# Optimization experiments

Hardware: AMD Instinct MI355X
Metric: run time of the kernel (lower is better)

## Reference

```python
import jax, jax.numpy as jnp
import numpy as np
from jax import lax

EMBED = 64


def setup_inputs() -> dict:
    key = jax.random.key(0)
    ks = jax.random.split(key, 5)
    b, l, v, e, h = 256, 1024, 96, 64, 256
    x = jax.random.randint(ks[0], (b, l), 0, v, dtype=jnp.int64)
    hidden = jnp.zeros((b, h), dtype=jnp.float32)
    # xavier-uniform-like init (scale by fan sums)
    emb = jax.random.normal(ks[1], (v, e), dtype=jnp.float32) * 0.1
    W_ih = jax.random.normal(ks[2], (e + h, h), dtype=jnp.float32) * (1.0 / np.sqrt(e + h))
    b_ih = jnp.zeros((h,), dtype=jnp.float32)
    W_ho = jax.random.normal(ks[3], (h, v), dtype=jnp.float32) * (1.0 / np.sqrt(h))
    b_ho = jnp.zeros((v,), dtype=jnp.float32)
    return {"x": x, "hidden": hidden, "emb": emb, "W_ih": W_ih, "b_ih": b_ih,
            "W_ho": W_ho, "b_ho": b_ho}


def reference(x, hidden, emb, W_ih, b_ih, W_ho, b_ho):
    # x: [b, l] int indices; hidden: [b, h]
    x_embed = emb[x]                      # [b, l, e]
    Wx, Wh = W_ih[:EMBED], W_ih[EMBED:]   # split cat([x, h]) @ W_ih
    # precompute input projections for all timesteps (batched GEMM)
    xproj = jnp.einsum('ble,eh->blh', x_embed, Wx) + b_ih  # [b, l, h]

    def step(h_prev, xp_t):
        h_t = jnp.tanh(xp_t + h_prev @ Wh)  # [b, h]
        return h_t, h_t

    final_hidden, hs = lax.scan(step, hidden, xproj.transpose(1, 0, 2))  # hs: [l, b, h]
    hs = hs.transpose(1, 0, 2)                     # [b, l, h]
    logits = jnp.einsum('blh,hv->blv', hs, W_ho) + b_ho  # [b, l, v]
    return logits, final_hidden
```

## Files before the change

kernel.cpp:

```cpp
#include <hip/hip_runtime.h>
#include <hip/hip_bf16.h>

#define Lv 1024
#define Vv 96
#define Ev 64
#define Hv 256
#define ROWS 16
#define HOFF (256 * 1024 * 96)
#define EPAD 72
#define HB 4096

typedef __attribute__((ext_vector_type(8))) short bf16x8;
typedef __attribute__((ext_vector_type(4))) float f32x4;
typedef __attribute__((ext_vector_type(2))) unsigned int u32x2;

__device__ __forceinline__ unsigned short f2b(float f) {
  unsigned u = __builtin_bit_cast(unsigned, f);
  return (unsigned short)((u + 0x7fffu + ((u >> 16) & 1u)) >> 16);
}
__device__ __forceinline__ unsigned cvtpk_bf16(float lo, float hi) {
  unsigned r;
  asm("v_cvt_pk_bf16_f32 %0, %1, %2" : "=v"(r) : "v"(lo), "v"(hi));
  return r;
}
__device__ __forceinline__ float fast_tanh(float x) {
  float e = __builtin_amdgcn_exp2f(x * 2.885390081777927f);
  return 1.0f - 2.0f * __builtin_amdgcn_rcpf(e + 1.0f);
}
__device__ __forceinline__ void step_barrier() {
  asm volatile("s_waitcnt lgkmcnt(0)\n\ts_barrier" ::: "memory");
  __builtin_amdgcn_sched_barrier(0);
}

__global__ void detect_i64(const int* __restrict__ x, int* __restrict__ flag) {
  if (threadIdx.x == 0 && blockIdx.x == 0) {
    int ok = 1;
    for (int i = 0; i < 64; ++i) ok &= (x[2 * i + 1] == 0);
    *flag = ok;
  }
}

__global__ __launch_bounds__(512, 2) void rnn8t(
    const int* __restrict__ x, const float* __restrict__ h0,
    const float* __restrict__ emb, const float* __restrict__ W_ih,
    const float* __restrict__ b_ih, float* __restrict__ out,
    unsigned short* __restrict__ hs, const int* __restrict__ flagp) {
  const int tid = threadIdx.x;
  const int w = tid >> 6, ln = tid & 63, lm = ln & 15, g = ln >> 4;
  const int r0 = blockIdx.x * ROWS;

  __shared__ __attribute__((aligned(16))) unsigned short s_h[2 * HB];
  __shared__ __attribute__((aligned(16))) unsigned short s_emb[Vv * EPAD];
  __shared__ unsigned char s_x[Lv * ROWS];

  const int flag = *flagp;

  for (int idx = tid; idx < Vv * Ev; idx += 512)
    s_emb[(idx >> 6) * EPAD + (idx & 63)] = f2b(emb[idx]);
  for (int idx = tid; idx < ROWS * Hv; idx += 512) {
    int b_ = idx >> 8, hd = idx & 255;
    s_h[HB + b_ * 256 + ((((hd >> 3) ^ (b_ & 7)) << 3) | (hd & 7))] =
        f2b(h0[(r0 + b_) * Hv + hd]);
  }
  for (int idx = tid; idx < ROWS * Lv; idx += 512) {
    int t = idx >> 4, row = idx & 15;
    long long src = (long long)(r0 + row) * Lv + t;
    int v = flag ? x[2 * src] : x[src];
    s_x[t * ROWS + row] = (unsigned char)v;
  }

  bf16x8 wh[2][8], wx[2][2];
  f32x4 bihv[2];
#pragma unroll
  for (int nt = 0; nt < 2; ++nt) {
    const int n = 32 * w + 16 * nt + lm;
#pragma unroll
    for (int kf = 0; kf < 8; ++kf)
#pragma unroll
      for (int i = 0; i < 8; ++i)
        wh[nt][kf][i] = (short)f2b(W_ih[(Ev + 32 * kf + 8 * g + i) * Hv + n]);
#pragma unroll
    for (int kf = 0; kf < 2; ++kf)
#pragma unroll
      for (int i = 0; i < 8; ++i)
        wx[nt][kf][i] = (short)f2b(W_ih[(32 * kf + 8 * g + i) * Hv + n]);
    bihv[nt] = *(const f32x4*)&b_ih[32 * w + 16 * nt + 4 * g];
  }

  const unsigned short* ra[8];
#pragma unroll
  for (int kf = 0; kf < 8; ++kf)
    ra[kf] = &s_h[lm * 256 + (((4 * kf + g) ^ (lm & 7)) << 3)];
  unsigned short* wa[2];
#pragma unroll
  for (int nt = 0; nt < 2; ++nt)
    wa[nt] = &s_h[lm * 256 + (((4 * w + 2 * nt + (g >> 1)) ^ (lm & 7)) << 3) +
                  ((g & 1) << 2)];
  unsigned short* hp = hs + (size_t)(r0 + lm) * 0 ;
  hp = hs + (size_t)(r0 + lm) * 256 + 32 * w + 4 * g;

  __syncthreads();

  bf16x8 ef0, ef1;
  int xi_n;
  {
    int xi0 = s_x[lm];
    const unsigned short* ep = &s_emb[xi0 * EPAD + 8 * g];
    ef0 = *(const bf16x8*)ep;
    ef1 = *(const bf16x8*)(ep + 32);
    xi_n = s_x[ROWS + lm];
  }

#define STEP(TT, RB, WB, LAST)                                                    \
  do {                                                                            \
    bf16x8 af[8];                                                                 \
    _Pragma("unroll") for (int kf = 0; kf < 8; ++kf)                              \
        af[kf] = *(const bf16x8*)(ra[kf] + (RB));                                 \
    f32x4 aA0 = bihv[0], aA1 = bihv[1];                                           \
    f32x4 aB0 = {0.f, 0.f, 0.f, 0.f}, aB1 = {0.f, 0.f, 0.f, 0.f};                 \
    aA0 = __builtin_amdgcn_mfma_f32_16x16x32_bf16(wx[0][0], ef0, aA0, 0, 0, 0);   \
    aA1 = __builtin_amdgcn_mfma_f32_16x16x32_bf16(wx[1][0], ef0, aA1, 0, 0, 0);   \
    aB0 = __builtin_amdgcn_mfma_f32_16x16x32_bf16(wx[0][1], ef1, aB0, 0, 0, 0);   \
    aB1 = __builtin_amdgcn_mfma_f32_16x16x32_bf16(wx[1][1], ef1, aB1, 0, 0, 0);   \
    _Pragma("unroll") for (int kf = 0; kf < 4; ++kf) {                            \
      aA0 = __builtin_amdgcn_mfma_f32_16x16x32_bf16(wh[0][kf], af[kf], aA0, 0, 0, 0); \
      aA1 = __builtin_amdgcn_mfma_f32_16x16x32_bf16(wh[1][kf], af[kf], aA1, 0, 0, 0); \
    }                                                                             \
    _Pragma("unroll") for (int kf = 4; kf < 8; ++kf) {                            \
      aB0 = __builtin_amdgcn_mfma_f32_16x16x32_bf16(wh[0][kf], af[kf], aB0, 0, 0, 0); \
      aB1 = __builtin_amdgcn_mfma_f32_16x16x32_bf16(wh[1][kf], af[kf], aB1, 0, 0, 0); \
    }                                                                             \
    {                                      \
      const unsigned short* ep = &s_emb[xi_n * EPAD + 8 * g];                     \
      ef0 = *(const bf16x8*)ep;                                                   \
      ef1 = *(const bf16x8*)(ep + 32);                                            \
      int tn = ((TT) + 2 < Lv) ? (TT) + 2 : (Lv - 1);                             \
      xi_n = s_x[tn * ROWS + lm];                                                 \
    }                                                                             \
    float h0v = fast_tanh(aA0[0] + aB0[0]), h1v = fast_tanh(aA0[1] + aB0[1]);     \
    float h2v = fast_tanh(aA0[2] + aB0[2]), h3v = fast_tanh(aA0[3] + aB0[3]);     \
    float h4v = fast_tanh(aA1[0] + aB1[0]), h5v = fast_tanh(aA1[1] + aB1[1]);     \
    float h6v = fast_tanh(aA1[2] + aB1[2]), h7v = fast_tanh(aA1[3] + aB1[3]);     \
    u32x2 p0, p1;                                                                 \
    p0[0] = cvtpk_bf16(h0v, h1v);                                                 \
    p0[1] = cvtpk_bf16(h2v, h3v);                                                 \
    p1[0] = cvtpk_bf16(h4v, h5v);                                                 \
    p1[1] = cvtpk_bf16(h6v, h7v);                                                 \
    *(u32x2*)(wa[0] + (WB)) = p0;                                                 \
    *(u32x2*)(wa[1] + (WB)) = p1;                                                 \
    *(u32x2*)hp = p0;                                           \
    *(u32x2*)(hp + 16) = p1;                                    \
    hp += 256 * 256;                                                              \
    if (LAST) {                                                                   \
      float* fo = out + HOFF + (size_t)(r0 + lm) * Hv + 32 * w + 4 * g;           \
      *(f32x4*)fo = (f32x4){h0v, h1v, h2v, h3v};                                  \
      *(f32x4*)(fo + 16) = (f32x4){h4v, h5v, h6v, h7v};                           \
    }                                                                             \
    step_barrier();                                                               \
  } while (0)

  STEP(0, HB, 0, 0);
  for (int t = 1; t < Lv - 1; t += 2) {
    STEP(t, 0, HB, 0);
    STEP(t + 1, HB, 0, 0);
  }
  STEP(Lv - 1, 0, HB, 1);
#undef STEP
}

__global__ __launch_bounds__(512, 2) void logits_gemm(
    const unsigned short* __restrict__ hs, const float* __restrict__ W_ho,
    const float* __restrict__ b_ho, float* __restrict__ out) {
  const int tid = threadIdx.x;
  const int w = tid >> 6, ln = tid & 63, lm = ln & 15, g = ln >> 4;
  const int tg = blockIdx.x >> 2, bg = blockIdx.x & 3;

  __shared__ __attribute__((aligned(16))) unsigned short s_who[3072 * 8];
  for (int f = tid; f < 3072; f += 512) {
    int vt = f >> 9, kf = (f >> 6) & 7, lane = f & 63;
    int k0 = 32 * kf + 8 * (lane >> 4), v = 16 * vt + (lane & 15);
    bf16x8 fr;
#pragma unroll
    for (int i = 0; i < 8; ++i) fr[i] = (short)f2b(W_ho[(k0 + i) * Vv + v]);
    *(bf16x8*)&s_who[f * 8] = fr;
  }
  __syncthreads();

  const int bt = w & 3, vg = w >> 2;
  const int b0 = bg * 64 + bt * 16;
  const int j0 = vg * 3;
  float bb[3];
#pragma unroll
  for (int jj = 0; jj < 3; ++jj) bb[jj] = b_ho[16 * (j0 + jj) + lm];

#pragma unroll
  for (int tt = 0; tt < 4; ++tt) {
    const int t = tg * 4 + tt;
    const unsigned short* hpb =
        hs + (size_t)t * (256 * 256) + (b0 + lm) * 256 + 8 * g;
    f32x4 acc[3];
#pragma unroll
    for (int jj = 0; jj < 3; ++jj)
      acc[jj] = (f32x4){bb[jj], bb[jj], bb[jj], bb[jj]};
#pragma unroll
    for (int kf = 0; kf < 8; ++kf) {
      bf16x8 af = *(const bf16x8*)(hpb + 32 * kf);
#pragma unroll
      for (int jj = 0; jj < 3; ++jj) {
        bf16x8 bw = *(const bf16x8*)&s_who[(((j0 + jj) * 8 + kf) * 64 + ln) * 8];
        acc[jj] =
            __builtin_amdgcn_mfma_f32_16x16x32_bf16(af, bw, acc[jj], 0, 0, 0);
      }
    }
#pragma unroll
    for (int jj = 0; jj < 3; ++jj)
#pragma unroll
      for (int rr = 0; rr < 4; ++rr)
        out[(size_t)(b0 + 4 * g + rr) * (Lv * Vv) + (size_t)t * Vv +
            16 * (j0 + jj) + lm] = acc[jj][rr];
  }
}

__global__ __launch_bounds__(512, 2) void rnn8(
    const int* __restrict__ x, const float* __restrict__ h0,
    const float* __restrict__ emb, const float* __restrict__ W_ih,
    const float* __restrict__ b_ih, const float* __restrict__ W_ho,
    const float* __restrict__ b_ho, float* __restrict__ out,
    const int* __restrict__ flagp) {
  const int tid = threadIdx.x;
  const int w = tid >> 6, ln = tid & 63, lm = ln & 15, g = ln >> 4;
  const int r0 = blockIdx.x * ROWS;

  __shared__ __attribute__((aligned(16))) unsigned short s_emb[Vv * EPAD];
  __shared__ __attribute__((aligned(16))) unsigned short s_h[2 * HB];
  __shared__ unsigned char s_x[Lv * ROWS];

  const int flag = *flagp;

  for (int idx = tid; idx < Vv * Ev; idx += 512)
    s_emb[(idx >> 6) * EPAD + (idx & 63)] = f2b(emb[idx]);
  for (int idx = tid; idx < ROWS * Hv; idx += 512) {
    int m = idx >> 8, nn = idx & 255;
    s_h[HB + (m << 8) + ((((nn >> 3) ^ (m & 7)) << 3) | (nn & 7))] =
        f2b(h0[(r0 + m) * Hv + nn]);
  }
  for (int idx = tid; idx < ROWS * Lv; idx += 512) {
    int row = idx >> 10, t = idx & 1023;
    long long src = (long long)(r0 + row) * Lv + t;
    int v = flag ? x[2 * src] : x[src];
    s_x[t * ROWS + row] = (unsigned char)v;
  }

  bf16x8 wh[2][8], wx[2][2], who[8];
  float bih[2], bhov = 0.0f;
#pragma unroll
  for (int nt = 0; nt < 2; ++nt) {
    const int n = 32 * w + 16 * nt + lm;
    bih[nt] = b_ih[n];
#pragma unroll
    for (int kf = 0; kf < 8; ++kf)
#pragma unroll
      for (int i = 0; i < 8; ++i)
        wh[nt][kf][i] = (short)f2b(W_ih[(Ev + 32 * kf + 8 * g + i) * Hv + n]);
#pragma unroll
    for (int kf = 0; kf < 2; ++kf)
#pragma unroll
      for (int i = 0; i < 8; ++i)
        wx[nt][kf][i] = (short)f2b(W_ih[(32 * kf + 8 * g + i) * Hv + n]);
  }
  if (w < 6) {
    const int n = 16 * w + lm;
    bhov = b_ho[n];
#pragma unroll
    for (int kf = 0; kf < 8; ++kf)
#pragma unroll
      for (int i = 0; i < 8; ++i)
        who[kf][i] = (short)f2b(W_ho[(32 * kf + 8 * g + i) * Vv + n]);
  }

  const unsigned short* ra[8];
#pragma unroll
  for (int kf = 0; kf < 8; ++kf)
    ra[kf] = &s_h[(lm << 8) + (((4 * kf + g) ^ (lm & 7)) << 3)];
  unsigned short* wa[8];
#pragma unroll
  for (int nt = 0; nt < 2; ++nt)
#pragma unroll
    for (int rr = 0; rr < 4; ++rr) {
      int m = 4 * g + rr, n = 32 * w + 16 * nt + lm;
      wa[nt * 4 + rr] = &s_h[(m << 8) + ((((n >> 3) ^ (m & 7)) << 3) | (n & 7))];
    }
  float* ob[4] = {out, out, out, out};
  if (w < 6) {
#pragma unroll
    for (int rr = 0; rr < 4; ++rr)
      ob[rr] = out + (size_t)(r0 + 4 * g + rr) * (Lv * Vv) + 16 * w + lm;
  }

  __syncthreads();

  bf16x8 ef0, ef1;
  {
    int xi = s_x[lm];
    const unsigned short* ep = &s_emb[xi * EPAD + 8 * g];
    ef0 = *(const bf16x8*)ep;
    ef1 = *(const bf16x8*)(ep + 32);
  }

#define STEP8(TT, RB, WB, DOLOG, LAST)                                             \
  do {                                                                             \
    bf16x8 af[8];                                                                  \
    _Pragma("unroll") for (int kf = 0; kf < 8; ++kf)                               \
        af[kf] = *(const bf16x8*)(ra[kf] + (RB));                                  \
    f32x4 a0 = {bih[0], bih[0], bih[0], bih[0]};                                   \
    f32x4 a1 = {bih[1], bih[1], bih[1], bih[1]};                                   \
    a0 = __builtin_amdgcn_mfma_f32_16x16x32_bf16(ef0, wx[0][0], a0, 0, 0, 0);      \
    a1 = __builtin_amdgcn_mfma_f32_16x16x32_bf16(ef0, wx[1][0], a1, 0, 0, 0);      \
    a0 = __builtin_amdgcn_mfma_f32_16x16x32_bf16(ef1, wx[0][1], a0, 0, 0, 0);      \
    a1 = __builtin_amdgcn_mfma_f32_16x16x32_bf16(ef1, wx[1][1], a1, 0, 0, 0);      \
    _Pragma("unroll") for (int kf = 0; kf < 8; ++kf) {                             \
      a0 = __builtin_amdgcn_mfma_f32_16x16x32_bf16(af[kf], wh[0][kf], a0, 0, 0, 0);\
      a1 = __builtin_amdgcn_mfma_f32_16x16x32_bf16(af[kf], wh[1][kf], a1, 0, 0, 0);\
    }                                                                              \
    if ((DOLOG) && w < 6) {                                                        \
      f32x4 l = {bhov, bhov, bhov, bhov};                                          \
      _Pragma("unroll") for (int kf = 0; kf < 8; ++kf)                             \
          l = __builtin_amdgcn_mfma_f32_16x16x32_bf16(af[kf], who[kf], l, 0, 0, 0);\
      const size_t o = (size_t)((TT)-1) * Vv;                                      \
      ob[0][o] = l[0]; ob[1][o] = l[1]; ob[2][o] = l[2]; ob[3][o] = l[3];          \
    }                                                                              \
    {                                                                              \
      int tn = ((TT) + 1 < Lv) ? (TT) + 1 : (Lv - 1);                              \
      int xi = s_x[tn * ROWS + lm];                                                \
      const unsigned short* ep = &s_emb[xi * EPAD + 8 * g];                        \
      ef0 = *(const bf16x8*)ep;                                                    \
      ef1 = *(const bf16x8*)(ep + 32);                                             \
    }                                                                              \
    float th0 = fast_tanh(a0[0]), th1 = fast_tanh(a0[1]);                          \
    float th2 = fast_tanh(a0[2]), th3 = fast_tanh(a0[3]);                          \
    float th4 = fast_tanh(a1[0]), th5 = fast_tanh(a1[1]);                          \
    float th6 = fast_tanh(a1[2]), th7 = fast_tanh(a1[3]);                          \
    unsigned p01 = cvtpk_bf16(th0, th1), p23 = cvtpk_bf16(th2, th3);               \
    unsigned p45 = cvtpk_bf16(th4, th5), p67 = cvtpk_bf16(th6, th7);               \
    wa[0][WB] = (unsigned short)p01;                                               \
    wa[1][WB] = (unsigned short)(p01 >> 16);                                       \
    wa[2][WB] = (unsigned short)p23;                                               \
    wa[3][WB] = (unsigned short)(p23 >> 16);                                       \
    wa[4][WB] = (unsigned short)p45;                                               \
    wa[5][WB] = (unsigned short)(p45 >> 16);                                       \
    wa[6][WB] = (unsigned short)p67;                                               \
    wa[7][WB] = (unsigned short)(p67 >> 16);                                       \
    if (LAST) {                                                                    \
      float* fh = out + HOFF + (size_t)(r0 + 4 * g) * Hv + 32 * w + lm;            \
      fh[0 * Hv] = th0; fh[1 * Hv] = th1; fh[2 * Hv] = th2; fh[3 * Hv] = th3;      \
      fh[0 * Hv + 16] = th4; fh[1 * Hv + 16] = th5;                                \
      fh[2 * Hv + 16] = th6; fh[3 * Hv + 16] = th7;                                \
    }                                                                              \
    asm volatile("s_waitcnt lgkmcnt(0)\n\ts_barrier" ::: "memory");                \
    __builtin_amdgcn_sched_barrier(0);                                             \
  } while (0)

  STEP8(0, HB, 0, 0, 0);
  for (int t = 1; t < Lv - 1; t += 2) {
    STEP8(t, 0, HB, 1, 0);
    STEP8(t + 1, HB, 0, 1, 0);
  }
  STEP8(Lv - 1, 0, HB, 1, 1);

  if (w < 6) {
    bf16x8 af[8];
#pragma unroll
    for (int kf = 0; kf < 8; ++kf) af[kf] = *(const bf16x8*)(ra[kf] + HB);
    f32x4 l = {bhov, bhov, bhov, bhov};
#pragma unroll
    for (int kf = 0; kf < 8; ++kf)
      l = __builtin_amdgcn_mfma_f32_16x16x32_bf16(af[kf], who[kf], l, 0, 0, 0);
    const size_t o = (size_t)(Lv - 1) * Vv;
    ob[0][o] = l[0]; ob[1][o] = l[1]; ob[2][o] = l[2]; ob[3][o] = l[3];
  }
#undef STEP8
}

extern "C" void kernel_launch(void* const* d_in, const int* in_sizes, int n_in,
                              void* d_out, int out_size, void* d_ws, size_t ws_size,
                              hipStream_t stream) {
  const int* x     = (const int*)d_in[0];
  const float* h0  = (const float*)d_in[1];
  const float* emb = (const float*)d_in[2];
  const float* Wih = (const float*)d_in[3];
  const float* bih = (const float*)d_in[4];
  const float* Who = (const float*)d_in[5];
  const float* bho = (const float*)d_in[6];
  float* out = (float*)d_out;
  int* flag = (int*)d_ws;

  const size_t hs_bytes = (size_t)Lv * 256 * 256 * 2;
  detect_i64<<<1, 64, 0, stream>>>(x, flag);
  if (ws_size >= hs_bytes + 256) {
    unsigned short* hsp = (unsigned short*)((char*)d_ws + 256);
    rnn8t<<<16, 512, 0, stream>>>(x, h0, emb, Wih, bih, out, hsp, flag);
    logits_gemm<<<1024, 512, 0, stream>>>(hsp, Who, bho, out);
  } else {
    rnn8<<<16, 512, 0, stream>>>(x, h0, emb, Wih, bih, Who, bho, out, flag);
  }
}
```

Measured before the change: 714.8 us.

## Split the recurrence across 64 blocks of 4 batch rows each

The recurrent kernel now handles 4 batch rows per block instead of 16, so 64 blocks run instead of 16 and more compute units take part. The MFMA tiles still cover 16 rows, so only the first 4 lanes' results are stored and the rest is wasted work. The MFMA chain is also split across four independent accumulators to shorten each step's dependency chain before tanh. The aim is to cut per-step latency on the serial critical path, at the cost of redundant matrix-unit work and more blocks each loading the full weights.

```diff
diff --git a/kernel.cpp b/kernel.cpp
--- a/kernel.cpp
+++ b/kernel.cpp
@@ -5,9 +5,11 @@
 #define Vv 96
 #define Ev 64
 #define Hv 256
+#define NB 4
 #define ROWS 16
 #define HOFF (256 * 1024 * 96)
 #define EPAD 72
+#define HBP 1024
 #define HB 4096
 
 typedef __attribute__((ext_vector_type(8))) short bf16x8;
@@ -40,33 +42,34 @@
   }
 }
 
-__global__ __launch_bounds__(512, 2) void rnn8t(
+__global__ __launch_bounds__(512, 2) void rnn4t(
     const int* __restrict__ x, const float* __restrict__ h0,
     const float* __restrict__ emb, const float* __restrict__ W_ih,
     const float* __restrict__ b_ih, float* __restrict__ out,
     unsigned short* __restrict__ hs, const int* __restrict__ flagp) {
   const int tid = threadIdx.x;
   const int w = tid >> 6, ln = tid & 63, lm = ln & 15, g = ln >> 4;
-  const int r0 = blockIdx.x * ROWS;
-
-  __shared__ __attribute__((aligned(16))) unsigned short s_h[2 * HB];
+  const int lmb = lm & (NB - 1);
+  const int r0 = blockIdx.x * NB;
+
+  __shared__ __attribute__((aligned(16))) unsigned short s_h[2 * HBP];
   __shared__ __attribute__((aligned(16))) unsigned short s_emb[Vv * EPAD];
-  __shared__ unsigned char s_x[Lv * ROWS];
+  __shared__ unsigned char s_x[Lv * NB];
 
   const int flag = *flagp;
 
   for (int idx = tid; idx < Vv * Ev; idx += 512)
     s_emb[(idx >> 6) * EPAD + (idx & 63)] = f2b(emb[idx]);
-  for (int idx = tid; idx < ROWS * Hv; idx += 512) {
+  for (int idx = tid; idx < NB * Hv; idx += 512) {
     int b_ = idx >> 8, hd = idx & 255;
-    s_h[HB + b_ * 256 + ((((hd >> 3) ^ (b_ & 7)) << 3) | (hd & 7))] =
+    s_h[HBP + b_ * 256 + ((((hd >> 3) ^ b_) << 3) | (hd & 7))] =
         f2b(h0[(r0 + b_) * Hv + hd]);
   }
-  for (int idx = tid; idx < ROWS * Lv; idx += 512) {
-    int t = idx >> 4, row = idx & 15;
+  for (int idx = tid; idx < NB * Lv; idx += 512) {
+    int t = idx >> 2, row = idx & (NB - 1);
     long long src = (long long)(r0 + row) * Lv + t;
     int v = flag ? x[2 * src] : x[src];
-    s_x[t * ROWS + row] = (unsigned char)v;
+    s_x[t * NB + row] = (unsigned char)v;
   }
 
   bf16x8 wh[2][8], wx[2][2];
@@ -90,25 +93,24 @@
   const unsigned short* ra[8];
 #pragma unroll
   for (int kf = 0; kf < 8; ++kf)
-    ra[kf] = &s_h[lm * 256 + (((4 * kf + g) ^ (lm & 7)) << 3)];
+    ra[kf] = &s_h[lmb * 256 + (((4 * kf + g) ^ lmb) << 3)];
   unsigned short* wa[2];
 #pragma unroll
   for (int nt = 0; nt < 2; ++nt)
-    wa[nt] = &s_h[lm * 256 + (((4 * w + 2 * nt + (g >> 1)) ^ (lm & 7)) << 3) +
+    wa[nt] = &s_h[lmb * 256 + (((4 * w + 2 * nt + (g >> 1)) ^ lmb) << 3) +
                   ((g & 1) << 2)];
-  unsigned short* hp = hs + (size_t)(r0 + lm) * 0 ;
-  hp = hs + (size_t)(r0 + lm) * 256 + 32 * w + 4 * g;
+  unsigned short* hp = hs + (size_t)(r0 + lmb) * 256 + 32 * w + 4 * g;
 
   __syncthreads();
 
   bf16x8 ef0, ef1;
   int xi_n;
   {
-    int xi0 = s_x[lm];
+    int xi0 = s_x[lmb];
     const unsigned short* ep = &s_emb[xi0 * EPAD + 8 * g];
     ef0 = *(const bf16x8*)ep;
     ef1 = *(const bf16x8*)(ep + 32);
-    xi_n = s_x[ROWS + lm];
+    xi_n = s_x[NB + lmb];
   }
 
 #define STEP(TT, RB, WB, LAST)                                                    \
@@ -116,55 +118,71 @@
     bf16x8 af[8];                                                                 \
     _Pragma("unroll") for (int kf = 0; kf < 8; ++kf)                              \
         af[kf] = *(const bf16x8*)(ra[kf] + (RB));                                 \
-    f32x4 aA0 = bihv[0], aA1 = bihv[1];                                           \
-    f32x4 aB0 = {0.f, 0.f, 0.f, 0.f}, aB1 = {0.f, 0.f, 0.f, 0.f};                 \
-    aA0 = __builtin_amdgcn_mfma_f32_16x16x32_bf16(wx[0][0], ef0, aA0, 0, 0, 0);   \
-    aA1 = __builtin_amdgcn_mfma_f32_16x16x32_bf16(wx[1][0], ef0, aA1, 0, 0, 0);   \
-    aB0 = __builtin_amdgcn_mfma_f32_16x16x32_bf16(wx[0][1], ef1, aB0, 0, 0, 0);   \
-    aB1 = __builtin_amdgcn_mfma_f32_16x16x32_bf16(wx[1][1], ef1, aB1, 0, 0, 0);   \
-    _Pragma("unroll") for (int kf = 0; kf < 4; ++kf) {                            \
-      aA0 = __builtin_amdgcn_mfma_f32_16x16x32_bf16(wh[0][kf], af[kf], aA0, 0, 0, 0); \
-      aA1 = __builtin_amdgcn_mfma_f32_16x16x32_bf16(wh[1][kf], af[kf], aA1, 0, 0, 0); \
-    }                                                                             \
-    _Pragma("unroll") for (int kf = 4; kf < 8; ++kf) {                            \
-      aB0 = __builtin_amdgcn_mfma_f32_16x16x32_bf16(wh[0][kf], af[kf], aB0, 0, 0, 0); \
-      aB1 = __builtin_amdgcn_mfma_f32_16x16x32_bf16(wh[1][kf], af[kf], aB1, 0, 0, 0); \
-    }                                                                             \
+                                                     \
+    f32x4 c00 = bihv[0], c01 = {0, 0, 0, 0}, c02 = {0, 0, 0, 0}, c03 = {0, 0, 0, 0}; \
+    f32x4 c10 = bihv[1], c11 = {0, 0, 0, 0}, c12 = {0, 0, 0, 0}, c13 = {0, 0, 0, 0}; \
+    c00 = __builtin_amdgcn_mfma_f32_16x16x32_bf16(wh[0][0], af[0], c00, 0, 0, 0); \
+    c10 = __builtin_amdgcn_mfma_f32_16x16x32_bf16(wh[1][0], af[0], c10, 0, 0, 0); \
+    c01 = __builtin_amdgcn_mfma_f32_16x16x32_bf16(wh[0][2], af[2], c01, 0, 0, 0); \
+    c11 = __builtin_amdgcn_mfma_f32_16x16x32_bf16(wh[1][2], af[2], c11, 0, 0, 0); \
+    c02 = __builtin_amdgcn_mfma_f32_16x16x32_bf16(wh[0][4], af[4], c02, 0, 0, 0); \
+    c12 = __builtin_amdgcn_mfma_f32_16x16x32_bf16(wh[1][4], af[4], c12, 0, 0, 0); \
+    c03 = __builtin_amdgcn_mfma_f32_16x16x32_bf16(wh[0][6], af[6], c03, 0, 0, 0); \
+    c13 = __builtin_amdgcn_mfma_f32_16x16x32_bf16(wh[1][6], af[6], c13, 0, 0, 0); \
+    c00 = __builtin_amdgcn_mfma_f32_16x16x32_bf16(wh[0][1], af[1], c00, 0, 0, 0); \
+    c10 = __builtin_amdgcn_mfma_f32_16x16x32_bf16(wh[1][1], af[1], c10, 0, 0, 0); \
+    c01 = __builtin_amdgcn_mfma_f32_16x16x32_bf16(wh[0][3], af[3], c01, 0, 0, 0); \
+    c11 = __builtin_amdgcn_mfma_f32_16x16x32_bf16(wh[1][3], af[3], c11, 0, 0, 0); \
+    c02 = __builtin_amdgcn_mfma_f32_16x16x32_bf16(wh[0][5], af[5], c02, 0, 0, 0); \
+    c12 = __builtin_amdgcn_mfma_f32_16x16x32_bf16(wh[1][5], af[5], c12, 0, 0, 0); \
+    c03 = __builtin_amdgcn_mfma_f32_16x16x32_bf16(wh[0][7], af[7], c03, 0, 0, 0); \
+    c13 = __builtin_amdgcn_mfma_f32_16x16x32_bf16(wh[1][7], af[7], c13, 0, 0, 0); \
+    c00 = __builtin_amdgcn_mfma_f32_16x16x32_bf16(wx[0][0], ef0, c00, 0, 0, 0);   \
+    c10 = __builtin_amdgcn_mfma_f32_16x16x32_bf16(wx[1][0], ef0, c10, 0, 0, 0);   \
+    c02 = __builtin_amdgcn_mfma_f32_16x16x32_bf16(wx[0][1], ef1, c02, 0, 0, 0);   \
+    c12 = __builtin_amdgcn_mfma_f32_16x16x32_bf16(wx[1][1], ef1, c12, 0, 0, 0);   \
     {                                      \
       const unsigned short* ep = &s_emb[xi_n * EPAD + 8 * g];                     \
       ef0 = *(const bf16x8*)ep;                                                   \
       ef1 = *(const bf16x8*)(ep + 32);                                            \
       int tn = ((TT) + 2 < Lv) ? (TT) + 2 : (Lv - 1);                             \
-      xi_n = s_x[tn * ROWS + lm];                                                 \
+      xi_n = s_x[tn * NB + lmb];                                                  \
     }                                                                             \
-    float h0v = fast_tanh(aA0[0] + aB0[0]), h1v = fast_tanh(aA0[1] + aB0[1]);     \
-    float h2v = fast_tanh(aA0[2] + aB0[2]), h3v = fast_tanh(aA0[3] + aB0[3]);     \
-    float h4v = fast_tanh(aA1[0] + aB1[0]), h5v = fast_tanh(aA1[1] + aB1[1]);     \
-    float h6v = fast_tanh(aA1[2] + aB1[2]), h7v = fast_tanh(aA1[3] + aB1[3]);     \
+    f32x4 s0, s1;                                                                 \
+    _Pragma("unroll") for (int rr = 0; rr < 4; ++rr) {                            \
+      s0[rr] = (c00[rr] + c01[rr]) + (c02[rr] + c03[rr]);                         \
+      s1[rr] = (c10[rr] + c11[rr]) + (c12[rr] + c13[rr]);                         \
+    }                                                                             \
+    float h0v = fast_tanh(s0[0]), h1v = fast_tanh(s0[1]);                         \
+    float h2v = fast_tanh(s0[2]), h3v = fast_tanh(s0[3]);                         \
+    float h4v = fast_tanh(s1[0]), h5v = fast_tanh(s1[1]);                         \
+    float h6v = fast_tanh(s1[2]), h7v = fast_tanh(s1[3]);                         \
     u32x2 p0, p1;                                                                 \
     p0[0] = cvtpk_bf16(h0v, h1v);                                                 \
     p0[1] = cvtpk_bf16(h2v, h3v);                                                 \
     p1[0] = cvtpk_bf16(h4v, h5v);                                                 \
     p1[1] = cvtpk_bf16(h6v, h7v);                                                 \
-    *(u32x2*)(wa[0] + (WB)) = p0;                                                 \
-    *(u32x2*)(wa[1] + (WB)) = p1;                                                 \
-    *(u32x2*)hp = p0;                                           \
-    *(u32x2*)(hp + 16) = p1;                                    \
+    if (lm < NB) {                                                                \
+      *(u32x2*)(wa[0] + (WB)) = p0;                                               \
+      *(u32x2*)(wa[1] + (WB)) = p1;                                               \
+      *(u32x2*)hp = p0;                                         \
+      *(u32x2*)(hp + 16) = p1;                                  \
+      if (LAST) {                                                                 \
+        float* fo = out + HOFF + (size_t)(r0 + lm) * Hv + 32 * w + 4 * g;         \
+        *(f32x4*)fo = (f32x4){h0v, h1v, h2v, h3v};                                \
+        *(f32x4*)(fo + 16) = (f32x4){h4v, h5v, h6v, h7v};                         \
+      }                                                                           \
+    }                                                                             \
     hp += 256 * 256;                                                              \
-    if (LAST) {                                                                   \
-      float* fo = out + HOFF + (size_t)(r0 + lm) * Hv + 32 * w + 4 * g;           \
-      *(f32x4*)fo = (f32x4){h0v, h1v, h2v, h3v};                                  \
-      *(f32x4*)(fo + 16) = (f32x4){h4v, h5v, h6v, h7v};                           \
-    }                                                                             \
     step_barrier();                                                               \
   } while (0)
 
-  STEP(0, HB, 0, 0);
+  STEP(0, HBP, 0, 0);
   for (int t = 1; t < Lv - 1; t += 2) {
-    STEP(t, 0, HB, 0);
-    STEP(t + 1, HB, 0, 0);
-  }
-  STEP(Lv - 1, 0, HB, 1);
+    STEP(t, 0, HBP, 0);
+    STEP(t + 1, HBP, 0, 0);
+  }
+  STEP(Lv - 1, 0, HBP, 1);
 #undef STEP
 }
 
@@ -398,7 +416,7 @@
   detect_i64<<<1, 64, 0, stream>>>(x, flag);
   if (ws_size >= hs_bytes + 256) {
     unsigned short* hsp = (unsigned short*)((char*)d_ws + 256);
-    rnn8t<<<16, 512, 0, stream>>>(x, h0, emb, Wih, bih, out, hsp, flag);
+    rnn4t<<<64, 512, 0, stream>>>(x, h0, emb, Wih, bih, out, hsp, flag);
     logits_gemm<<<1024, 512, 0, stream>>>(hsp, Who, bho, out);
   } else {
     rnn8<<<16, 512, 0, stream>>>(x, h0, emb, Wih, bih, Who, bho, out, flag);
```

After: 796.6 us. 11.4% more time.
